# Kernel optimization log

Measured on AMD Instinct MI355X. Metric: run time of the kernel, lower is better.

Reference implementation:

```python
import jax, jax.numpy as jnp
import numpy as np

# ranges from init_kwargs
T2P_RANGE = (1.0, 500.0)
B1_RANGE = (0.2, 1.6)

NX, NY = 256, 256
NUM_T2S, NUM_B1S, ETL = 100, 30, 16


def _nan_to_num0(x):
    # torch.nan_to_num(x, nan=0.0, posinf=0.0); inputs here are non-negative so
    # neginf never occurs, but we zero it too for safety.
    return jnp.nan_to_num(x, nan=0.0, posinf=0.0, neginf=0.0)


def setup_inputs() -> dict:
    key = jax.random.key(0)
    k1, k2, k3 = jax.random.split(key, 3)
    slice_signal = jax.random.uniform(k1, (NX, NY, ETL), dtype=jnp.float32)
    db_mag = jax.random.uniform(k2, (NUM_T2S, NUM_B1S, ETL), dtype=jnp.float32)
    db_t2s_ms = jnp.linspace(1.0, 1000.0, NUM_T2S, dtype=jnp.float32)
    db_b1s = jnp.linspace(0.2, 1.6, NUM_B1S, dtype=jnp.float32)
    delta_t_t2p_ms = 9.0 * jnp.arange(1, ETL + 1, dtype=jnp.float32)  # echo times
    estimates = jax.random.uniform(k3, (2, NX, NY), dtype=jnp.float32)
    return {
        "slice_signal": slice_signal,
        "db_mag": db_mag,
        "db_t2s_ms": db_t2s_ms,
        "db_b1s": db_b1s,
        "delta_t_t2p_ms": delta_t_t2p_ms,
        "estimates": estimates,
    }


def reference(slice_signal, db_mag, db_t2s_ms, db_b1s, delta_t_t2p_ms, estimates):
    etl = slice_signal.shape[-1]
    sig = _nan_to_num0(slice_signal / jnp.linalg.norm(slice_signal, axis=-1, keepdims=True))
    sig = sig.reshape(-1, etl)  # (P, etl)

    # b1 map from estimates[1], scaled to b1_range
    b1 = B1_RANGE[0] + (B1_RANGE[1] - B1_RANGE[0]) * estimates[1]  # (nx, ny)
    # TV term: torch.gradient default == numpy.gradient (central diff interior,
    # one-sided edges)
    g0, g1 = jnp.gradient(b1)
    f_2 = jnp.sum(jnp.abs(g0) + jnp.abs(g1))

    # nearest-neighbor B1 dictionary lookup (non-differentiable gather)
    b1_flat = b1.reshape(-1)  # (P,)
    b1_idx = jnp.argmin((b1_flat[:, None] - db_b1s[None, :]) ** 2, axis=-1)  # (P,)
    db = db_mag[:, b1_idx]  # (T2, P, etl)

    # eta = exp(-dt / t2p), t2p from estimates[0] scaled to t2p_range
    t2p = T2P_RANGE[0] + (T2P_RANGE[1] - T2P_RANGE[0]) * estimates[0].reshape(-1)  # (P,)
    eta = jnp.exp(-delta_t_t2p_ms[None, :] / t2p[:, None])  # (P, etl)

    s_db = db * eta[None]  # (T2, P, etl)
    s_db = _nan_to_num0(s_db / jnp.linalg.norm(s_db, axis=-1, keepdims=True))

    l2_min = jnp.linalg.norm(s_db - sig[None], axis=-1)  # (T2, P)
    f_1 = jnp.sum(jnp.linalg.norm(l2_min, axis=-1))  # sum over T2 of per-T2 norms over pixels
    return f_1 + f_2
```

## Files before the change

### kernel.cpp

```cpp
#include <hip/hip_runtime.h>
#include <math.h>

constexpr int NXc = 256, NYc = 256, ETLc = 16, NTc = 100, NBc = 30;
constexpr int NPIX = NXc * NYc;
constexpr int TCHUNK = 10;
constexpr int NCHUNK = 10;
constexpr int RSTRIDE = 20;
constexpr int P2STRIDE = 132;


__global__ __launch_bounds__(256) void k_main(
    const float* __restrict__ sig,
    const float* __restrict__ db_mag,
    const float* __restrict__ dtt,
    const float* __restrict__ est,
    float* __restrict__ ws_f1,
    float* __restrict__ ws_f2)
{
    const int tid    = threadIdx.x;
    const int pixblk = blockIdx.x & 255;
    const int tchunk = blockIdx.x >> 8;
    const int p = (pixblk << 8) | tid;
    const int x = p >> 8;
    const int y = p & 255;
    const int t0 = tchunk * TCHUNK;
    const int wid = tid >> 6, lane = tid & 63;

    alignas(16) __shared__ float lds[TCHUNK * NBc * RSTRIDE];
    __shared__ float s_p[TCHUNK * P2STRIDE];
    __shared__ float s_f2[4];

    const float4* gsrc = reinterpret_cast<const float4*>(db_mag + (size_t)t0 * (NBc * ETLc));
    for (int i = tid; i < TCHUNK * 120; i += 256) {
        const int ttl = i / 120;
        const int rem = i - ttl * 120;
        const int jbl = rem >> 2;
        const int k   = rem & 3;
        float4 v = gsrc[i];
        *reinterpret_cast<float4*>(&lds[ttl * (NBc * RSTRIDE) + jbl * RSTRIDE + k * 4]) = v;
    }

    const float4* sp = reinterpret_cast<const float4*>(sig + (size_t)p * ETLc);
    float s[16];
    {
        float4 a = sp[0], b = sp[1], c = sp[2], d = sp[3];
        s[0]=a.x; s[1]=a.y; s[2]=a.z;  s[3]=a.w;
        s[4]=b.x; s[5]=b.y; s[6]=b.z;  s[7]=b.w;
        s[8]=c.x; s[9]=c.y; s[10]=c.z; s[11]=c.w;
        s[12]=d.x; s[13]=d.y; s[14]=d.z; s[15]=d.w;
    }
    float snrm2 = 0.f;
#pragma unroll
    for (int e = 0; e < 16; ++e) snrm2 = fmaf(s[e], s[e], snrm2);
    const float sig2  = (snrm2 > 0.f) ? 1.0f : 0.0f;
    const float srinv = (snrm2 > 0.f) ? __builtin_amdgcn_rsqf(snrm2) : 0.0f;
    float sgn[16];
#pragma unroll
    for (int e = 0; e < 16; ++e) sgn[e] = s[e] * srinv;

    const float est0 = est[p];
    const float t2p  = 1.0f + 499.0f * est0;
    const float nrcp = -__builtin_amdgcn_rcpf(t2p);
    float eta[16];
#pragma unroll
    for (int e = 0; e < 16; ++e) eta[e] = __expf(dtt[e] * nrcp);

    const float est1 = est[NPIX + p];
    float kf = roundf(est1 * 29.0f);
    kf = fminf(fmaxf(kf, 0.0f), 29.0f);
    const int jb = (int)kf;

    __syncthreads();

#pragma unroll 2
    for (int tt = 0; tt < TCHUNK; ++tt) {
        const float4* lp = reinterpret_cast<const float4*>(
            &lds[tt * (NBc * RSTRIDE) + jb * RSTRIDE]);
        float4 a = lp[0], b = lp[1], c = lp[2], d = lp[3];
        float dbr[16];
        dbr[0]=a.x; dbr[1]=a.y; dbr[2]=a.z;  dbr[3]=a.w;
        dbr[4]=b.x; dbr[5]=b.y; dbr[6]=b.z;  dbr[7]=b.w;
        dbr[8]=c.x; dbr[9]=c.y; dbr[10]=c.z; dbr[11]=c.w;
        dbr[12]=d.x; dbr[13]=d.y; dbr[14]=d.z; dbr[15]=d.w;

        float nrm2 = 0.f, dotv = 0.f;
#pragma unroll
        for (int e = 0; e < 16; ++e) {
            float v = dbr[e] * eta[e];
            nrm2 = fmaf(v, v, nrm2);
            dotv = fmaf(v, sgn[e], dotv);
        }
        float l2sq;
        if (nrm2 > 0.f) l2sq = sig2 + 1.0f - 2.0f * dotv * __builtin_amdgcn_rsqf(nrm2);
        else            l2sq = sig2;
        float r = (l2sq < 0.f) ? 0.f : l2sq;

        r += __shfl_xor(r, 1, 64);
        if ((lane & 1) == 0)
            s_p[tt * P2STRIDE + (wid << 5) + (lane >> 1)] = r;
    }
    __syncthreads();

    if (tid < TCHUNK * 16) {
        const int t = tid >> 4, j = tid & 15;
        const float* row = &s_p[t * P2STRIDE + j];
        float b = 0.f;
#pragma unroll
        for (int k = 0; k < 8; ++k) b += row[k * 16];
        b += __shfl_xor(b, 1, 64);
        b += __shfl_xor(b, 2, 64);
        b += __shfl_xor(b, 4, 64);
        b += __shfl_xor(b, 8, 64);
        if (j == 0) ws_f1[(size_t)(t0 + t) * 256 + pixblk] = b;
    }

    if (tchunk == 0) {
        const float* e1 = est + NPIX;
        const float b1 = 0.2f + 1.4f * est1;
        float g0, g1;
        {
            float c = b1;
            if (x == 0)            g0 = (0.2f + 1.4f * e1[p + 256]) - c;
            else if (x == NXc - 1) g0 = c - (0.2f + 1.4f * e1[p - 256]);
            else                   g0 = 0.5f * ((0.2f + 1.4f * e1[p + 256]) - (0.2f + 1.4f * e1[p - 256]));
            if (y == 0)            g1 = (0.2f + 1.4f * e1[p + 1]) - c;
            else if (y == NYc - 1) g1 = c - (0.2f + 1.4f * e1[p - 1]);
            else                   g1 = 0.5f * ((0.2f + 1.4f * e1[p + 1]) - (0.2f + 1.4f * e1[p - 1]));
        }
        float r = fabsf(g0) + fabsf(g1);
#pragma unroll
        for (int m = 32; m; m >>= 1) r += __shfl_xor(r, m, 64);
        if (lane == 0) s_f2[wid] = r;
        __syncthreads();
        if (tid == 0) ws_f2[pixblk] = s_f2[0] + s_f2[1] + s_f2[2] + s_f2[3];
    }
}

__global__ __launch_bounds__(512) void k_final(
    const float* __restrict__ ws_f1,
    const float* __restrict__ ws_f2,
    float* __restrict__ out)
{
    const int tid = threadIdx.x;
    const int t = tid >> 2, g = tid & 3;
    float sum = 0.f;
    if (t < NTc) {
        const float4* p4 = reinterpret_cast<const float4*>(ws_f1 + (size_t)t * 256 + g * 64);
#pragma unroll
        for (int i = 0; i < 16; ++i) { float4 v = p4[i]; sum += (v.x + v.y) + (v.z + v.w); }
    }
    sum += __shfl_xor(sum, 1, 64);
    sum += __shfl_xor(sum, 2, 64);

    __shared__ float s_sq[128];
    if (tid < 128) s_sq[tid] = 0.f;
    __syncthreads();
    if (g == 0 && t < NTc) s_sq[t] = sqrtf(sum);
    __syncthreads();

    if (tid < 64) {
        float v = s_sq[tid] + s_sq[tid + 64];
        v += (ws_f2[tid] + ws_f2[tid + 64]) + (ws_f2[tid + 128] + ws_f2[tid + 192]);
#pragma unroll
        for (int m = 32; m; m >>= 1) v += __shfl_xor(v, m, 64);
        if (tid == 0) out[0] = v;
    }
}

extern "C" void kernel_launch(void* const* d_in, const int* in_sizes, int n_in,
                              void* d_out, int out_size, void* d_ws, size_t ws_size,
                              hipStream_t stream) {
    const float* sig    = (const float*)d_in[0];
    const float* db_mag = (const float*)d_in[1];
    const float* dtt    = (const float*)d_in[4];
    const float* est    = (const float*)d_in[5];
    float* out = (float*)d_out;

    float* ws_f1 = (float*)d_ws;
    float* ws_f2 = ws_f1 + (size_t)NTc * 256;

    k_main <<<dim3(256 * NCHUNK), dim3(256), 0, stream>>>(sig, db_mag, dtt, est, ws_f1, ws_f2);
    k_final<<<dim3(1),            dim3(512), 0, stream>>>(ws_f1, ws_f2, out);
}
```

Baseline: 24.09 us.

## Process two T2 chunks per block with bf16-packed dictionary in LDS

Halves the grid so each block handles two T2 chunks, reusing the per-pixel signal load, normalization and eta computation across 20 T2 values instead of 10. The dictionary slice is packed to bf16 in LDS, halving LDS footprint and read traffic, and the second chunk's load is overlapped with the first chunk's reduction. Launch bounds request 4 blocks per SIMD. The bf16 rounding of db_mag loosens precision of the result.

```diff
diff --git a/kernel.cpp b/kernel.cpp
--- a/kernel.cpp
+++ b/kernel.cpp
@@ -4,12 +4,17 @@
 constexpr int NXc = 256, NYc = 256, ETLc = 16, NTc = 100, NBc = 30;
 constexpr int NPIX = NXc * NYc;
 constexpr int TCHUNK = 10;
-constexpr int NCHUNK = 10;
-constexpr int RSTRIDE = 20;
+constexpr int NSUPER = 5;
+constexpr int R32 = 12;
 constexpr int P2STRIDE = 132;
 
-
-__global__ __launch_bounds__(256) void k_main(
+__device__ __forceinline__ unsigned pack2bf(float lo, float hi) {
+    unsigned bl = __float_as_uint(lo), bh = __float_as_uint(hi);
+    return ((bl + 0x8000u) >> 16) | ((bh + 0x8000u) & 0xffff0000u);
+}
+
+
+__global__ __launch_bounds__(256, 4) void k_main(
     const float* __restrict__ sig,
     const float* __restrict__ db_mag,
     const float* __restrict__ dtt,
@@ -19,25 +24,32 @@
 {
     const int tid    = threadIdx.x;
     const int pixblk = blockIdx.x & 255;
-    const int tchunk = blockIdx.x >> 8;
+    const int sch    = blockIdx.x >> 8;
     const int p = (pixblk << 8) | tid;
     const int x = p >> 8;
     const int y = p & 255;
-    const int t0 = tchunk * TCHUNK;
+    const int t0a = sch * (2 * TCHUNK);
+    const int t0b = t0a + TCHUNK;
     const int wid = tid >> 6, lane = tid & 63;
 
-    alignas(16) __shared__ float lds[TCHUNK * NBc * RSTRIDE];
+    alignas(16) __shared__ unsigned lds32[TCHUNK * NBc * R32];
     __shared__ float s_p[TCHUNK * P2STRIDE];
     __shared__ float s_f2[4];
 
-    const float4* gsrc = reinterpret_cast<const float4*>(db_mag + (size_t)t0 * (NBc * ETLc));
-    for (int i = tid; i < TCHUNK * 120; i += 256) {
-        const int ttl = i / 120;
-        const int rem = i - ttl * 120;
-        const int jbl = rem >> 2;
-        const int k   = rem & 3;
-        float4 v = gsrc[i];
-        *reinterpret_cast<float4*>(&lds[ttl * (NBc * RSTRIDE) + jbl * RSTRIDE + k * 4]) = v;
+    {
+        const float4* gsrc = reinterpret_cast<const float4*>(db_mag + (size_t)t0a * (NBc * ETLc));
+        for (int i = tid; i < TCHUNK * 60; i += 256) {
+            const int t = i / 60;
+            const int rem = i - t * 60;
+            const int jbl = rem >> 1;
+            const int h   = rem & 1;
+            const float4* g = gsrc + ((t * NBc + jbl) * 4 + h * 2);
+            float4 A = g[0], B = g[1];
+            uint4 w;
+            w.x = pack2bf(A.x, A.y); w.y = pack2bf(A.z, A.w);
+            w.z = pack2bf(B.x, B.y); w.w = pack2bf(B.z, B.w);
+            *reinterpret_cast<uint4*>(&lds32[(t * NBc + jbl) * R32 + h * 4]) = w;
+        }
     }
 
     const float4* sp = reinterpret_cast<const float4*>(sig + (size_t)p * ETLc);
@@ -70,70 +82,105 @@
     kf = fminf(fmaxf(kf, 0.0f), 29.0f);
     const int jb = (int)kf;
 
-    __syncthreads();
-
-#pragma unroll 2
-    for (int tt = 0; tt < TCHUNK; ++tt) {
-        const float4* lp = reinterpret_cast<const float4*>(
-            &lds[tt * (NBc * RSTRIDE) + jb * RSTRIDE]);
-        float4 a = lp[0], b = lp[1], c = lp[2], d = lp[3];
-        float dbr[16];
-        dbr[0]=a.x; dbr[1]=a.y; dbr[2]=a.z;  dbr[3]=a.w;
-        dbr[4]=b.x; dbr[5]=b.y; dbr[6]=b.z;  dbr[7]=b.w;
-        dbr[8]=c.x; dbr[9]=c.y; dbr[10]=c.z; dbr[11]=c.w;
-        dbr[12]=d.x; dbr[13]=d.y; dbr[14]=d.z; dbr[15]=d.w;
-
-        float nrm2 = 0.f, dotv = 0.f;
-#pragma unroll
-        for (int e = 0; e < 16; ++e) {
-            float v = dbr[e] * eta[e];
-            nrm2 = fmaf(v, v, nrm2);
-            dotv = fmaf(v, sgn[e], dotv);
-        }
-        float l2sq;
-        if (nrm2 > 0.f) l2sq = sig2 + 1.0f - 2.0f * dotv * __builtin_amdgcn_rsqf(nrm2);
-        else            l2sq = sig2;
-        float r = (l2sq < 0.f) ? 0.f : l2sq;
-
-        r += __shfl_xor(r, 1, 64);
-        if ((lane & 1) == 0)
-            s_p[tt * P2STRIDE + (wid << 5) + (lane >> 1)] = r;
-    }
-    __syncthreads();
-
-    if (tid < TCHUNK * 16) {
-        const int t = tid >> 4, j = tid & 15;
-        const float* row = &s_p[t * P2STRIDE + j];
-        float b = 0.f;
-#pragma unroll
-        for (int k = 0; k < 8; ++k) b += row[k * 16];
-        b += __shfl_xor(b, 1, 64);
-        b += __shfl_xor(b, 2, 64);
-        b += __shfl_xor(b, 4, 64);
-        b += __shfl_xor(b, 8, 64);
-        if (j == 0) ws_f1[(size_t)(t0 + t) * 256 + pixblk] = b;
-    }
-
-    if (tchunk == 0) {
+    if (sch == 0) {
         const float* e1 = est + NPIX;
-        const float b1 = 0.2f + 1.4f * est1;
+        const float c = 0.2f + 1.4f * est1;
         float g0, g1;
-        {
-            float c = b1;
-            if (x == 0)            g0 = (0.2f + 1.4f * e1[p + 256]) - c;
-            else if (x == NXc - 1) g0 = c - (0.2f + 1.4f * e1[p - 256]);
-            else                   g0 = 0.5f * ((0.2f + 1.4f * e1[p + 256]) - (0.2f + 1.4f * e1[p - 256]));
-            if (y == 0)            g1 = (0.2f + 1.4f * e1[p + 1]) - c;
-            else if (y == NYc - 1) g1 = c - (0.2f + 1.4f * e1[p - 1]);
-            else                   g1 = 0.5f * ((0.2f + 1.4f * e1[p + 1]) - (0.2f + 1.4f * e1[p - 1]));
-        }
+        if (x == 0)            g0 = (0.2f + 1.4f * e1[p + 256]) - c;
+        else if (x == NXc - 1) g0 = c - (0.2f + 1.4f * e1[p - 256]);
+        else                   g0 = 0.5f * ((0.2f + 1.4f * e1[p + 256]) - (0.2f + 1.4f * e1[p - 256]));
+        if (y == 0)            g1 = (0.2f + 1.4f * e1[p + 1]) - c;
+        else if (y == NYc - 1) g1 = c - (0.2f + 1.4f * e1[p - 1]);
+        else                   g1 = 0.5f * ((0.2f + 1.4f * e1[p + 1]) - (0.2f + 1.4f * e1[p - 1]));
         float r = fabsf(g0) + fabsf(g1);
 #pragma unroll
         for (int m = 32; m; m >>= 1) r += __shfl_xor(r, m, 64);
         if (lane == 0) s_f2[wid] = r;
-        __syncthreads();
-        if (tid == 0) ws_f2[pixblk] = s_f2[0] + s_f2[1] + s_f2[2] + s_f2[3];
-    }
+    }
+
+    __syncthreads();
+    if (sch == 0 && tid == 0) ws_f2[pixblk] = s_f2[0] + s_f2[1] + s_f2[2] + s_f2[3];
+
+#define TLOOP(T0)                                                               \
+    _Pragma("unroll 4")                                                         \
+    for (int tt = 0; tt < TCHUNK; ++tt) {                                       \
+        const uint4* lp = reinterpret_cast<const uint4*>(                       \
+            &lds32[tt * (NBc * R32) + jb * R32]);                               \
+        uint4 q0 = lp[0], q1 = lp[1];                                           \
+        float dbr[16];                                                          \
+        dbr[0]  = __uint_as_float(q0.x << 16);                                  \
+        dbr[1]  = __uint_as_float(q0.x & 0xffff0000u);                          \
+        dbr[2]  = __uint_as_float(q0.y << 16);                                  \
+        dbr[3]  = __uint_as_float(q0.y & 0xffff0000u);                          \
+        dbr[4]  = __uint_as_float(q0.z << 16);                                  \
+        dbr[5]  = __uint_as_float(q0.z & 0xffff0000u);                          \
+        dbr[6]  = __uint_as_float(q0.w << 16);                                  \
+        dbr[7]  = __uint_as_float(q0.w & 0xffff0000u);                          \
+        dbr[8]  = __uint_as_float(q1.x << 16);                                  \
+        dbr[9]  = __uint_as_float(q1.x & 0xffff0000u);                          \
+        dbr[10] = __uint_as_float(q1.y << 16);                                  \
+        dbr[11] = __uint_as_float(q1.y & 0xffff0000u);                          \
+        dbr[12] = __uint_as_float(q1.z << 16);                                  \
+        dbr[13] = __uint_as_float(q1.z & 0xffff0000u);                          \
+        dbr[14] = __uint_as_float(q1.w << 16);                                  \
+        dbr[15] = __uint_as_float(q1.w & 0xffff0000u);                          \
+        float nrm2 = 0.f, dotv = 0.f;                                           \
+        _Pragma("unroll")                                                       \
+        for (int e = 0; e < 16; ++e) {                                          \
+            float v = dbr[e] * eta[e];                                          \
+            nrm2 = fmaf(v, v, nrm2);                                            \
+            dotv = fmaf(v, sgn[e], dotv);                                       \
+        }                                                                       \
+        float l2sq;                                                             \
+        if (nrm2 > 0.f) l2sq = sig2 + 1.0f - 2.0f * dotv * __builtin_amdgcn_rsqf(nrm2); \
+        else            l2sq = sig2;                                            \
+        float r = (l2sq < 0.f) ? 0.f : l2sq;                                    \
+        r += __shfl_xor(r, 1, 64);                                              \
+        if ((lane & 1) == 0)                                                    \
+            s_p[tt * P2STRIDE + (wid << 5) + (lane >> 1)] = r;                  \
+    }
+
+#define FINISH(T0)                                                              \
+    if (tid < TCHUNK * 16) {                                                    \
+        const int t = tid >> 4, j = tid & 15;                                   \
+        const float* row = &s_p[t * P2STRIDE + j];                              \
+        float b = 0.f;                                                          \
+        _Pragma("unroll")                                                       \
+        for (int k = 0; k < 8; ++k) b += row[k * 16];                           \
+        b += __shfl_xor(b, 1, 64);                                              \
+        b += __shfl_xor(b, 2, 64);                                              \
+        b += __shfl_xor(b, 4, 64);                                              \
+        b += __shfl_xor(b, 8, 64);                                              \
+        if (j == 0) ws_f1[(size_t)((T0) + t) * 256 + pixblk] = b;               \
+    }
+
+    TLOOP(t0a)
+    __syncthreads();
+
+    {
+        const float4* gsrc = reinterpret_cast<const float4*>(db_mag + (size_t)t0b * (NBc * ETLc));
+        for (int i = tid; i < TCHUNK * 60; i += 256) {
+            const int t = i / 60;
+            const int rem = i - t * 60;
+            const int jbl = rem >> 1;
+            const int h   = rem & 1;
+            const float4* g = gsrc + ((t * NBc + jbl) * 4 + h * 2);
+            float4 A = g[0], B = g[1];
+            uint4 w;
+            w.x = pack2bf(A.x, A.y); w.y = pack2bf(A.z, A.w);
+            w.z = pack2bf(B.x, B.y); w.w = pack2bf(B.z, B.w);
+            *reinterpret_cast<uint4*>(&lds32[(t * NBc + jbl) * R32 + h * 4]) = w;
+        }
+    }
+    FINISH(t0a)
+    __syncthreads();
+
+    TLOOP(t0b)
+    __syncthreads();
+    FINISH(t0b)
+
+#undef TLOOP
+#undef FINISH
 }
 
 __global__ __launch_bounds__(512) void k_final(
@@ -179,6 +226,6 @@
     float* ws_f1 = (float*)d_ws;
     float* ws_f2 = ws_f1 + (size_t)NTc * 256;
 
-    k_main <<<dim3(256 * NCHUNK), dim3(256), 0, stream>>>(sig, db_mag, dtt, est, ws_f1, ws_f2);
+    k_main <<<dim3(256 * NSUPER), dim3(256), 0, stream>>>(sig, db_mag, dtt, est, ws_f1, ws_f2);
     k_final<<<dim3(1),            dim3(512), 0, stream>>>(ws_f1, ws_f2, out);
 }
```

New measurement: 26.47 us. 9.9% more time.

## Use 1024-thread blocks with 8 uneven T2 chunks and fold TV gradient earlier

Applied to the files above, without the earlier changes.

Reorganizes the main kernel from 2560 blocks of 256 threads over 10 T2 chunks into 512 blocks of 1024 threads over 8 chunks of 12–13 T2 values. This cuts the redundant per-pixel signal normalization and eta exponentials, which are recomputed once per chunk, and reduces the number of dictionary LDS fills. The TV gradient reduction is moved before the main barrier, removing a separate synchronization. In exchange, large blocks with only two per CU may hurt latency hiding and load balance.

```diff
diff --git a/kernel.cpp b/kernel.cpp
--- a/kernel.cpp
+++ b/kernel.cpp
@@ -3,13 +3,13 @@
 
 constexpr int NXc = 256, NYc = 256, ETLc = 16, NTc = 100, NBc = 30;
 constexpr int NPIX = NXc * NYc;
-constexpr int TCHUNK = 10;
-constexpr int NCHUNK = 10;
+constexpr int TMAX = 13;
 constexpr int RSTRIDE = 20;
-constexpr int P2STRIDE = 132;
+constexpr int PST = 532;
+constexpr int QST = 132;
 
 
-__global__ __launch_bounds__(256) void k_main(
+__global__ __launch_bounds__(1024, 8) void k_main(
     const float* __restrict__ sig,
     const float* __restrict__ db_mag,
     const float* __restrict__ dtt,
@@ -17,27 +17,28 @@
     float* __restrict__ ws_f1,
     float* __restrict__ ws_f2)
 {
-    const int tid    = threadIdx.x;
-    const int pixblk = blockIdx.x & 255;
-    const int tchunk = blockIdx.x >> 8;
-    const int p = (pixblk << 8) | tid;
+    const int tid      = threadIdx.x;
+    const int pixgroup = blockIdx.x & 63;
+    const int tc       = blockIdx.x >> 6;
+    const int p = (pixgroup << 10) | tid;
     const int x = p >> 8;
     const int y = p & 255;
-    const int t0 = tchunk * TCHUNK;
-    const int wid = tid >> 6, lane = tid & 63;
+    const int t0   = (tc < 4) ? tc * 13 : 52 + (tc - 4) * 12;
+    const int tcnt = (tc < 4) ? 13 : 12;
+    const int lane = tid & 63;
 
-    alignas(16) __shared__ float lds[TCHUNK * NBc * RSTRIDE];
-    __shared__ float s_p[TCHUNK * P2STRIDE];
-    __shared__ float s_f2[4];
+    alignas(16) __shared__ float lds[TMAX * NBc * RSTRIDE];
+    __shared__ float s_p[TMAX * PST];
+    __shared__ float s_f2[16];
 
-    const float4* gsrc = reinterpret_cast<const float4*>(db_mag + (size_t)t0 * (NBc * ETLc));
-    for (int i = tid; i < TCHUNK * 120; i += 256) {
-        const int ttl = i / 120;
-        const int rem = i - ttl * 120;
-        const int jbl = rem >> 2;
-        const int k   = rem & 3;
-        float4 v = gsrc[i];
-        *reinterpret_cast<float4*>(&lds[ttl * (NBc * RSTRIDE) + jbl * RSTRIDE + k * 4]) = v;
+    {
+        const float4* gsrc = reinterpret_cast<const float4*>(db_mag + (size_t)t0 * (NBc * ETLc));
+        for (int i = tid; i < tcnt * 120; i += 1024) {
+            const int ttl = i / 120;
+            const int rem = i - ttl * 120;
+            *reinterpret_cast<float4*>(
+                &lds[ttl * (NBc * RSTRIDE) + (rem >> 2) * RSTRIDE + (rem & 3) * 4]) = gsrc[i];
+        }
     }
 
     const float4* sp = reinterpret_cast<const float4*>(sig + (size_t)p * ETLc);
@@ -70,10 +71,29 @@
     kf = fminf(fmaxf(kf, 0.0f), 29.0f);
     const int jb = (int)kf;
 
+    if (tc == 0) {
+        const float* e1 = est + NPIX;
+        const float c = 0.2f + 1.4f * est1;
+        float g0, g1;
+        if (x == 0)            g0 = (0.2f + 1.4f * e1[p + 256]) - c;
+        else if (x == NXc - 1) g0 = c - (0.2f + 1.4f * e1[p - 256]);
+        else                   g0 = 0.5f * ((0.2f + 1.4f * e1[p + 256]) - (0.2f + 1.4f * e1[p - 256]));
+        if (y == 0)            g1 = (0.2f + 1.4f * e1[p + 1]) - c;
+        else if (y == NYc - 1) g1 = c - (0.2f + 1.4f * e1[p - 1]);
+        else                   g1 = 0.5f * ((0.2f + 1.4f * e1[p + 1]) - (0.2f + 1.4f * e1[p - 1]));
+        float r = fabsf(g0) + fabsf(g1);
+#pragma unroll
+        for (int m = 32; m; m >>= 1) r += __shfl_xor(r, m, 64);
+        if (lane == 0) s_f2[tid >> 6] = r;
+    }
+
     __syncthreads();
+    if (tc == 0 && tid < 4)
+        ws_f2[(pixgroup << 2) + tid] =
+            (s_f2[tid*4+0] + s_f2[tid*4+1]) + (s_f2[tid*4+2] + s_f2[tid*4+3]);
 
-#pragma unroll 2
-    for (int tt = 0; tt < TCHUNK; ++tt) {
+#pragma unroll 1
+    for (int tt = 0; tt < tcnt; ++tt) {
         const float4* lp = reinterpret_cast<const float4*>(
             &lds[tt * (NBc * RSTRIDE) + jb * RSTRIDE]);
         float4 a = lp[0], b = lp[1], c = lp[2], d = lp[3];
@@ -97,13 +117,15 @@
 
         r += __shfl_xor(r, 1, 64);
         if ((lane & 1) == 0)
-            s_p[tt * P2STRIDE + (wid << 5) + (lane >> 1)] = r;
+            s_p[tt * PST + (tid >> 8) * QST + ((tid >> 1) & 127)] = r;
     }
     __syncthreads();
 
-    if (tid < TCHUNK * 16) {
-        const int t = tid >> 4, j = tid & 15;
-        const float* row = &s_p[t * P2STRIDE + j];
+    if (tid < tcnt * 64) {
+        const int t = tid >> 6;
+        const int q = (tid >> 4) & 3;
+        const int j = tid & 15;
+        const float* row = &s_p[t * PST + q * QST + j];
         float b = 0.f;
 #pragma unroll
         for (int k = 0; k < 8; ++k) b += row[k * 16];
@@ -111,28 +133,7 @@
         b += __shfl_xor(b, 2, 64);
         b += __shfl_xor(b, 4, 64);
         b += __shfl_xor(b, 8, 64);
-        if (j == 0) ws_f1[(size_t)(t0 + t) * 256 + pixblk] = b;
-    }
-
-    if (tchunk == 0) {
-        const float* e1 = est + NPIX;
-        const float b1 = 0.2f + 1.4f * est1;
-        float g0, g1;
-        {
-            float c = b1;
-            if (x == 0)            g0 = (0.2f + 1.4f * e1[p + 256]) - c;
-            else if (x == NXc - 1) g0 = c - (0.2f + 1.4f * e1[p - 256]);
-            else                   g0 = 0.5f * ((0.2f + 1.4f * e1[p + 256]) - (0.2f + 1.4f * e1[p - 256]));
-            if (y == 0)            g1 = (0.2f + 1.4f * e1[p + 1]) - c;
-            else if (y == NYc - 1) g1 = c - (0.2f + 1.4f * e1[p - 1]);
-            else                   g1 = 0.5f * ((0.2f + 1.4f * e1[p + 1]) - (0.2f + 1.4f * e1[p - 1]));
-        }
-        float r = fabsf(g0) + fabsf(g1);
-#pragma unroll
-        for (int m = 32; m; m >>= 1) r += __shfl_xor(r, m, 64);
-        if (lane == 0) s_f2[wid] = r;
-        __syncthreads();
-        if (tid == 0) ws_f2[pixblk] = s_f2[0] + s_f2[1] + s_f2[2] + s_f2[3];
+        if (j == 0) ws_f1[(size_t)(t0 + t) * 256 + (pixgroup << 2) + q] = b;
     }
 }
 
@@ -179,6 +180,6 @@
     float* ws_f1 = (float*)d_ws;
     float* ws_f2 = ws_f1 + (size_t)NTc * 256;
 
-    k_main <<<dim3(256 * NCHUNK), dim3(256), 0, stream>>>(sig, db_mag, dtt, est, ws_f1, ws_f2);
-    k_final<<<dim3(1),            dim3(512), 0, stream>>>(ws_f1, ws_f2, out);
+    k_main <<<dim3(64 * 8), dim3(1024), 0, stream>>>(sig, db_mag, dtt, est, ws_f1, ws_f2);
+    k_final<<<dim3(1),      dim3(512),  0, stream>>>(ws_f1, ws_f2, out);
 }
```

New measurement: 23.39 us. 1.03x faster.
